# Kernel optimization log

Measured on AMD Instinct MI355X. Metric: run time of the kernel, lower is better.

## Reference

```python
import jax, jax.numpy as jnp
import numpy as np

D_MODEL = 1024
NUM_LAYERS = 4
D_STATE = 64
D_CONV = 4
EXPAND = 2
HEADDIM = 64  # headdim = d_state per the module
D_INNER = EXPAND * D_MODEL              # 2048
NHEADS = D_INNER // HEADDIM             # 32
CONV_DIM = D_INNER + 2 * D_STATE        # 2176 (x, B, C)
D_IN_PROJ = 2 * D_INNER + 2 * D_STATE + NHEADS  # 4384 (z, xBC, dt)
EPS = 1e-5


def setup_inputs() -> dict:
    key = jax.random.key(0)
    ks = jax.random.split(key, 8)
    B, L = 4, 2048
    x = jax.random.normal(ks[0], (B, L, D_MODEL), dtype=jnp.float32)
    # stacked per-layer parameters
    in_w = jax.random.normal(ks[1], (NUM_LAYERS, D_MODEL, D_IN_PROJ), dtype=jnp.float32) * 0.02
    conv_w = (jax.random.uniform(ks[2], (NUM_LAYERS, D_CONV, CONV_DIM), dtype=jnp.float32) - 0.5) * (2.0 / np.sqrt(D_CONV))
    conv_b = jnp.zeros((NUM_LAYERS, CONV_DIM), dtype=jnp.float32)
    # dt init as in mamba-ssm: dt ~ exp(U * (log(0.1)-log(0.001)) + log(0.001)), dt_bias = inv_softplus(dt)
    u = jax.random.uniform(ks[3], (NUM_LAYERS, NHEADS), dtype=jnp.float32)
    dt = jnp.exp(u * (np.log(0.1) - np.log(0.001)) + np.log(0.001))
    dt_bias = dt + jnp.log(-jnp.expm1(-dt))
    A_log = jnp.log(jax.random.uniform(ks[4], (NUM_LAYERS, NHEADS), dtype=jnp.float32, minval=1.0, maxval=16.0))
    Dp = jnp.ones((NUM_LAYERS, NHEADS), dtype=jnp.float32)
    norm_w = jnp.ones((NUM_LAYERS, D_INNER), dtype=jnp.float32)
    out_w = jax.random.normal(ks[5], (NUM_LAYERS, D_INNER, D_MODEL), dtype=jnp.float32) * 0.02
    ln_w = jnp.ones((NUM_LAYERS, D_MODEL), dtype=jnp.float32)
    ln_b = jnp.zeros((NUM_LAYERS, D_MODEL), dtype=jnp.float32)
    return {"x": x, "ln_w": ln_w, "ln_b": ln_b, "in_w": in_w, "conv_w": conv_w,
            "conv_b": conv_b, "dt_bias": dt_bias, "A_log": A_log, "Dp": Dp,
            "norm_w": norm_w, "out_w": out_w}


def _layernorm(x, w, b):
    mu = jnp.mean(x, axis=-1, keepdims=True)
    xc = x - mu
    var = jnp.mean(xc * xc, axis=-1, keepdims=True)
    return xc * jax.lax.rsqrt(var + EPS) * w + b


def _mamba2(x, in_w, conv_w, conv_b, dt_bias, A_log, Dp, norm_w, out_w):
    Bb, L, _ = x.shape
    zxbcdt = jnp.einsum('bld,de->ble', x, in_w)            # (B,L,D_IN_PROJ)
    z = zxbcdt[..., :D_INNER]                               # (B,L,D_INNER)
    xBC = zxbcdt[..., D_INNER:D_INNER + CONV_DIM]           # (B,L,CONV_DIM)
    dt = jax.nn.softplus(zxbcdt[..., -NHEADS:] + dt_bias)   # (B,L,H)
    # causal depthwise conv1d (kernel D_CONV) + SiLU
    xp = jnp.pad(xBC, ((0, 0), (D_CONV - 1, 0), (0, 0)))
    conv = conv_b + sum(xp[:, k:k + L, :] * conv_w[k] for k in range(D_CONV))
    xBC = jax.nn.silu(conv)
    xs = xBC[..., :D_INNER].reshape(Bb, L, NHEADS, HEADDIM)  # (B,L,H,P)
    Bm = xBC[..., D_INNER:D_INNER + D_STATE]                 # (B,L,N), ngroups=1
    Cm = xBC[..., D_INNER + D_STATE:]                        # (B,L,N)
    A = -jnp.exp(A_log)                                      # (H,)
    dA = jnp.exp(dt * A)                                     # (B,L,H) decay per step
    dBx = dt[..., None] * xs                                 # (B,L,H,P)
    # selective state-space scan: h_t = dA_t*h_{t-1} + dBx_t (x) B_t ; y_t = h_t . C_t
    def step(h, t_in):
        dA_t, dBx_t, B_t, C_t = t_in
        h = h * dA_t[:, :, None, None] + dBx_t[..., None] * B_t[:, None, None, :]
        y = jnp.einsum('bhpn,bn->bhp', h, C_t)
        return h, y
    h0 = jnp.zeros((Bb, NHEADS, HEADDIM, D_STATE), x.dtype)
    xsT = (jnp.moveaxis(dA, 1, 0), jnp.moveaxis(dBx, 1, 0),
           jnp.moveaxis(Bm, 1, 0), jnp.moveaxis(Cm, 1, 0))
    _, yT = jax.lax.scan(step, h0, xsT)
    y = jnp.moveaxis(yT, 0, 1)                               # (B,L,H,P)
    y = y + Dp[None, None, :, None] * xs                     # skip via per-head D
    y = y.reshape(Bb, L, D_INNER)
    # gated RMSNorm (norm_before_gate=False): rmsnorm(y * silu(z)) * w
    y = y * jax.nn.silu(z)
    y = y * jax.lax.rsqrt(jnp.mean(y * y, axis=-1, keepdims=True) + EPS) * norm_w
    return jnp.einsum('ble,ed->bld', y, out_w)


def reference(x, ln_w, ln_b, in_w, conv_w, conv_b, dt_bias, A_log, Dp, norm_w, out_w):
    for i in range(NUM_LAYERS):
        xn = _layernorm(x, ln_w[i], ln_b[i])
        x = x + _mamba2(xn, in_w[i], conv_w[i], conv_b[i], dt_bias[i],
                        A_log[i], Dp[i], norm_w[i], out_w[i])
    return x
```

## Files before the change

kernel.cpp:

```cpp
#include <hip/hip_runtime.h>
#include <math.h>

#define LSEQ   2048
#define NROWS  8192
#define DMODEL 1024
#define DINNER 2048
#define NH     32
#define CONVD  2176
#define NPROJ  4256
#define NPROJ_PAD 4352
#define EPSV   1e-5f
#define SEGS   16
#define TSEG   128

typedef __bf16 bf16x8_t __attribute__((ext_vector_type(8)));
typedef float f32x4_t __attribute__((ext_vector_type(4)));
typedef unsigned short u16x8_t __attribute__((ext_vector_type(8)));

__device__ __forceinline__ unsigned short f2bf(float f) {
  unsigned int u = __float_as_uint(f);
  u += 0x7fffu + ((u >> 16) & 1u);
  return (unsigned short)(u >> 16);
}
__device__ __forceinline__ float bf2f(unsigned short u) {
  return __uint_as_float((unsigned int)u << 16);
}
__device__ __forceinline__ float siluf(float x) { return x / (1.f + expf(-x)); }

__device__ __forceinline__ void gload16(const unsigned short* g, unsigned short* l) {
  __builtin_amdgcn_global_load_lds(
      (const __attribute__((address_space(1))) void*)g,
      (__attribute__((address_space(3))) void*)l, 16, 0, 0);
}

__global__ __launch_bounds__(256) void ln_kernel(const float* __restrict__ X,
    const float* __restrict__ w, const float* __restrict__ b,
    unsigned short* __restrict__ out)
{
  const int r = blockIdx.x, tid = threadIdx.x;
  __shared__ float red[4];
  const float4 v = ((const float4*)(X + (size_t)r * DMODEL))[tid];
  float s = v.x + v.y + v.z + v.w;
#pragma unroll
  for (int o = 32; o > 0; o >>= 1) s += __shfl_down(s, o);
  if ((tid & 63) == 0) red[tid >> 6] = s;
  __syncthreads();
  const float mu = (red[0] + red[1] + red[2] + red[3]) * (1.f / DMODEL);
  __syncthreads();
  const float dx = v.x - mu, dy = v.y - mu, dz = v.z - mu, dw = v.w - mu;
  float ss = dx * dx + dy * dy + dz * dz + dw * dw;
#pragma unroll
  for (int o = 32; o > 0; o >>= 1) ss += __shfl_down(ss, o);
  if ((tid & 63) == 0) red[tid >> 6] = ss;
  __syncthreads();
  const float var = (red[0] + red[1] + red[2] + red[3]) * (1.f / DMODEL);
  const float rs = rsqrtf(var + EPSV);
  const float4 wv = ((const float4*)w)[tid];
  const float4 bv = ((const float4*)b)[tid];
  const size_t d = (size_t)r * DMODEL + tid * 4;
  out[d + 0] = f2bf(dx * rs * wv.x + bv.x);
  out[d + 1] = f2bf(dy * rs * wv.y + bv.y);
  out[d + 2] = f2bf(dz * rs * wv.z + bv.z);
  out[d + 3] = f2bf(dw * rs * wv.w + bv.w);
}

__global__ void transpose_bf16(const float* __restrict__ W,
    unsigned short* __restrict__ WT, int K, int N)
{
  __shared__ float t[32][33];
  const int n0 = blockIdx.x * 32, k0 = blockIdx.y * 32;
  const int tx = threadIdx.x, ty = threadIdx.y;
  if (n0 + tx < N) t[ty][tx] = W[(size_t)(k0 + ty) * N + n0 + tx];
  __syncthreads();
  if (n0 + ty < N) WT[(size_t)(n0 + ty) * K + k0 + tx] = f2bf(t[tx][ty]);
}

__global__ __launch_bounds__(256) void gemm_bf16(
    const unsigned short* __restrict__ A,
    const unsigned short* __restrict__ BT,
    float* __restrict__ Cf,
    unsigned short* __restrict__ Cb,
    int N, int K, int ldc)
{
  __shared__ unsigned short sA[128 * 32];
  __shared__ unsigned short sB[128 * 32];
  const int tid = threadIdx.x;
  const int w = tid >> 6, l = tid & 63;
  const int wr = w >> 1, wc = w & 1;
  const int la = l & 15, lb = l >> 4;
  const int m0 = blockIdx.x * 128, n0 = blockIdx.y * 128;
  f32x4_t acc[4][4];
#pragma unroll
  for (int i = 0; i < 4; ++i)
#pragma unroll
    for (int j = 0; j < 4; ++j) acc[i][j] = (f32x4_t){0.f, 0.f, 0.f, 0.f};

  const int r0 = tid >> 2, q0 = tid & 3;
  const unsigned short* Ag = A + (size_t)(m0 + r0) * K + q0 * 8;
  const unsigned short* Bg = BT + (size_t)(n0 + r0) * K + q0 * 8;

  for (int kt = 0; kt < K; kt += 32) {
    __syncthreads();
    gload16(Ag + kt,                   sA + tid * 8);
    gload16(Ag + (size_t)64 * K + kt,  sA + 2048 + tid * 8);
    gload16(Bg + kt,                   sB + tid * 8);
    gload16(Bg + (size_t)64 * K + kt,  sB + 2048 + tid * 8);
    __syncthreads();
    bf16x8_t af[4], bfr[4];
#pragma unroll
    for (int mi = 0; mi < 4; ++mi)
      af[mi] = *(const bf16x8_t*)(sA + (wr * 64 + mi * 16 + la) * 32 + lb * 8);
#pragma unroll
    for (int ni = 0; ni < 4; ++ni)
      bfr[ni] = *(const bf16x8_t*)(sB + (wc * 64 + ni * 16 + la) * 32 + lb * 8);
#pragma unroll
    for (int mi = 0; mi < 4; ++mi)
#pragma unroll
      for (int ni = 0; ni < 4; ++ni)
        acc[mi][ni] = __builtin_amdgcn_mfma_f32_16x16x32_bf16(af[mi], bfr[ni], acc[mi][ni], 0, 0, 0);
  }
#pragma unroll
  for (int mi = 0; mi < 4; ++mi) {
#pragma unroll
    for (int ni = 0; ni < 4; ++ni) {
      const int col = n0 + wc * 64 + ni * 16 + la;
      if (col < N) {
#pragma unroll
        for (int r = 0; r < 4; ++r) {
          const int row = m0 + wr * 64 + mi * 16 + lb * 4 + r;
          const size_t idx = (size_t)row * ldc + col;
          const float v = acc[mi][ni][r];
          if (Cb) Cb[idx] = f2bf(v);
          else    Cf[idx] += v;
        }
      }
    }
  }
}

__global__ __launch_bounds__(256) void conv_kernel(const unsigned short* __restrict__ zx,
    const float* __restrict__ cw, const float* __restrict__ cb,
    unsigned short* __restrict__ out)
{
  const int c8 = (blockIdx.x * 256 + threadIdx.x) * 8;
  if (c8 >= CONVD) return;
  const int r = blockIdx.y;
  const int l = r & (LSEQ - 1);
  float acc[8];
  {
    const float4 b0 = *(const float4*)(cb + c8);
    const float4 b1 = *(const float4*)(cb + c8 + 4);
    acc[0] = b0.x; acc[1] = b0.y; acc[2] = b0.z; acc[3] = b0.w;
    acc[4] = b1.x; acc[5] = b1.y; acc[6] = b1.z; acc[7] = b1.w;
  }
#pragma unroll
  for (int k = 0; k < 4; ++k) {
    if (l + k - 3 >= 0) {
      const u16x8_t v = *(const u16x8_t*)(zx + (size_t)(r + k - 3) * NPROJ + DINNER + c8);
      const float4 w0 = *(const float4*)(cw + k * CONVD + c8);
      const float4 w1 = *(const float4*)(cw + k * CONVD + c8 + 4);
      acc[0] = fmaf(bf2f(v[0]), w0.x, acc[0]);
      acc[1] = fmaf(bf2f(v[1]), w0.y, acc[1]);
      acc[2] = fmaf(bf2f(v[2]), w0.z, acc[2]);
      acc[3] = fmaf(bf2f(v[3]), w0.w, acc[3]);
      acc[4] = fmaf(bf2f(v[4]), w1.x, acc[4]);
      acc[5] = fmaf(bf2f(v[5]), w1.y, acc[5]);
      acc[6] = fmaf(bf2f(v[6]), w1.z, acc[6]);
      acc[7] = fmaf(bf2f(v[7]), w1.w, acc[7]);
    }
  }
  u16x8_t o;
#pragma unroll
  for (int j = 0; j < 8; ++j) o[j] = f2bf(siluf(acc[j]));
  *(u16x8_t*)(out + (size_t)r * CONVD + c8) = o;
}

#define CBB(t, cbyte)  ((char*)CB  + (t) * 256 + ((cbyte) ^ (((t) & 7) << 4)))
#define XTB(p, cbyte)  ((char*)Xt  + (p) * 256 + ((cbyte) ^ (((p) & 7) << 4)))
#define BTWB(n, cbyte) ((char*)Btw + (n) * 256 + ((cbyte) ^ (((n) & 7) << 4)))
__global__ __launch_bounds__(256) void ssd_chunk_kernel(
    const unsigned short* __restrict__ xbc,
    const unsigned short* __restrict__ zraw,
    const float* __restrict__ dt_bias,
    const float* __restrict__ A_log,
    const float* __restrict__ Dp,
    unsigned short* __restrict__ y, int ldy,
    unsigned short* __restrict__ H,
    float* __restrict__ cumdec)
{
  __shared__ unsigned short CB[TSEG * 128];
  __shared__ unsigned short Xt[64 * TSEG];
  __shared__ unsigned short Btw[64 * TSEG];
  __shared__ float cumS[TSEG], dtS[TSEG], wS[TSEG];
  const int id = blockIdx.x;
  const int bh = id >> 4, ch = id & 15;
  const int b = bh >> 5, h = bh & 31;
  const int tid = threadIdx.x;
  const int w = tid >> 6, l = tid & 63;
  const int la = l & 15, lb = l >> 4;
  const size_t row0 = (size_t)b * LSEQ + (size_t)ch * TSEG;
  const unsigned short* xr = xbc + row0 * CONVD;
  const float dp = Dp[h];

  {
    const int t = tid >> 1, q = tid & 1;
    const unsigned short* src = xr + (size_t)t * CONVD;
#pragma unroll
    for (int j = 0; j < 4; ++j) {
      const int c0 = q * 32 + j * 8;
      *(u16x8_t*)CBB(t, c0 * 2)       = *(const u16x8_t*)(src + 2112 + c0);
      *(u16x8_t*)CBB(t, 128 + c0 * 2) = *(const u16x8_t*)(src + 2048 + c0);
      const u16x8_t xv = *(const u16x8_t*)(src + h * 64 + c0);
#pragma unroll
      for (int e = 0; e < 8; ++e)
        *(unsigned short*)XTB(c0 + e, t * 2) = xv[e];
    }
  }
  if (w == 0) {
    const float bias = dt_bias[h];
    const float aexp = __expf(A_log[h]);
    const float x0 = bf2f(zraw[(row0 + l) * NPROJ + (DINNER + CONVD) + h]) + bias;
    const float x1 = bf2f(zraw[(row0 + 64 + l) * NPROJ + (DINNER + CONVD) + h]) + bias;
    const float d0 = (x0 > 20.f) ? x0 : log1pf(__expf(x0));
    const float d1 = (x1 > 20.f) ? x1 : log1pf(__expf(x1));
    float a0 = -d0 * aexp;
    float a1 = -d1 * aexp;
#pragma unroll
    for (int o = 1; o < 64; o <<= 1) { const float u = __shfl_up(a0, o); if (l >= o) a0 += u; }
    const float tot0 = __shfl(a0, 63);
#pragma unroll
    for (int o = 1; o < 64; o <<= 1) { const float u = __shfl_up(a1, o); if (l >= o) a1 += u; }
    a1 += tot0;
    const float cT = __shfl(a1, 63);
    cumS[l] = a0;       cumS[64 + l] = a1;
    dtS[l] = d0;        dtS[64 + l] = d1;
    wS[l] = __expf(cT - a0) * d0;
    wS[64 + l] = __expf(cT - a1) * d1;
    float* cdg = cumdec + (size_t)bh * LSEQ + (size_t)ch * TSEG;
    cdg[l] = __expf(a0);
    cdg[64 + l] = __expf(a1);
  }
  __syncthreads();

  f32x4_t g[2][8];
#pragma unroll
  for (int mi = 0; mi < 2; ++mi)
#pragma unroll
    for (int ni = 0; ni < 8; ++ni) g[mi][ni] = (f32x4_t){0.f, 0.f, 0.f, 0.f};
#pragma unroll
  for (int ks = 0; ks < 2; ++ks) {
    bf16x8_t af[2], bfr[8];
#pragma unroll
    for (int mi = 0; mi < 2; ++mi)
      af[mi] = *(const bf16x8_t*)CBB(w * 32 + mi * 16 + la, ks * 64 + lb * 16);
#pragma unroll
    for (int ni = 0; ni < 8; ++ni)
      bfr[ni] = *(const bf16x8_t*)CBB(ni * 16 + la, 128 + ks * 64 + lb * 16);
#pragma unroll
    for (int mi = 0; mi < 2; ++mi)
#pragma unroll
      for (int ni = 0; ni < 8; ++ni)
        g[mi][ni] = __builtin_amdgcn_mfma_f32_16x16x32_bf16(af[mi], bfr[ni], g[mi][ni], 0, 0, 0);
  }
  __syncthreads();

#pragma unroll
  for (int mi = 0; mi < 2; ++mi) {
#pragma unroll
    for (int ni = 0; ni < 8; ++ni) {
      const int s = ni * 16 + la;
#pragma unroll
      for (int r = 0; r < 4; ++r) {
        const int t = w * 32 + mi * 16 + lb * 4 + r;
        float mv = 0.f;
        if (s <= t) mv = g[mi][ni][r] * __expf(cumS[t] - cumS[s]) * dtS[s];
        if (s == t) mv += dp;
        *(unsigned short*)CBB(t, s * 2) = f2bf(mv);
      }
    }
  }
  {
    const int s = tid >> 1, q = tid & 1;
    const unsigned short* src = xr + (size_t)s * CONVD + 2048;
    const float ww = wS[s];
#pragma unroll
    for (int j = 0; j < 4; ++j) {
      const int c0 = q * 32 + j * 8;
      const u16x8_t bv = *(const u16x8_t*)(src + c0);
#pragma unroll
      for (int e = 0; e < 8; ++e)
        *(unsigned short*)BTWB(c0 + e, s * 2) = f2bf(bf2f(bv[e]) * ww);
    }
  }
  __syncthreads();

  f32x4_t y1[2][4];
#pragma unroll
  for (int mi = 0; mi < 2; ++mi)
#pragma unroll
    for (int ni = 0; ni < 4; ++ni) y1[mi][ni] = (f32x4_t){0.f, 0.f, 0.f, 0.f};
#pragma unroll
  for (int ks = 0; ks < 4; ++ks) {
    bf16x8_t af[2], xf[4];
#pragma unroll
    for (int mi = 0; mi < 2; ++mi)
      af[mi] = *(const bf16x8_t*)CBB(w * 32 + mi * 16 + la, ks * 64 + lb * 16);
#pragma unroll
    for (int ni = 0; ni < 4; ++ni)
      xf[ni] = *(const bf16x8_t*)XTB(ni * 16 + la, ks * 64 + lb * 16);
#pragma unroll
    for (int mi = 0; mi < 2; ++mi)
#pragma unroll
      for (int ni = 0; ni < 4; ++ni)
        y1[mi][ni] = __builtin_amdgcn_mfma_f32_16x16x32_bf16(af[mi], xf[ni], y1[mi][ni], 0, 0, 0);
  }
  f32x4_t hacc[4];
#pragma unroll
  for (int ni = 0; ni < 4; ++ni) hacc[ni] = (f32x4_t){0.f, 0.f, 0.f, 0.f};
#pragma unroll
  for (int ks = 0; ks < 4; ++ks) {
    const bf16x8_t af = *(const bf16x8_t*)XTB(w * 16 + la, ks * 64 + lb * 16);
    bf16x8_t bw[4];
#pragma unroll
    for (int ni = 0; ni < 4; ++ni)
      bw[ni] = *(const bf16x8_t*)BTWB(ni * 16 + la, ks * 64 + lb * 16);
#pragma unroll
    for (int ni = 0; ni < 4; ++ni)
      hacc[ni] = __builtin_amdgcn_mfma_f32_16x16x32_bf16(af, bw[ni], hacc[ni], 0, 0, 0);
  }

  unsigned short* yg = y + row0 * ldy + h * 64;
#pragma unroll
  for (int mi = 0; mi < 2; ++mi)
#pragma unroll
    for (int ni = 0; ni < 4; ++ni)
#pragma unroll
      for (int r = 0; r < 4; ++r) {
        const int t = w * 32 + mi * 16 + lb * 4 + r;
        yg[(size_t)t * ldy + ni * 16 + la] = f2bf(y1[mi][ni][r]);
      }
  unsigned short* Hg = H + ((size_t)ch * 128 + bh) * 4096;
#pragma unroll
  for (int ni = 0; ni < 4; ++ni)
#pragma unroll
    for (int r = 0; r < 4; ++r) {
      const int p = w * 16 + lb * 4 + r;
      Hg[p * 64 + ni * 16 + la] = f2bf(hacc[ni][r]);
    }
}

__global__ __launch_bounds__(256) void scan2_kernel(
    unsigned short* __restrict__ H, const float* __restrict__ cumdec)
{
  const int bh = blockIdx.x;
  const int e = threadIdx.x * 16;
  float hs[16];
#pragma unroll
  for (int k = 0; k < 16; ++k) hs[k] = 0.f;
  unsigned short* Hb = H + (size_t)bh * 4096 + e;
  const float* cd = cumdec + (size_t)bh * LSEQ;
  for (int s = 0; s < SEGS; ++s) {
    unsigned short* p = Hb + (size_t)s * 128 * 4096;
    const float rseg = cd[s * TSEG + TSEG - 1];
    u16x8_t v0 = *(u16x8_t*)p, v1 = *(u16x8_t*)(p + 8);
    u16x8_t w0, w1;
#pragma unroll
    for (int k = 0; k < 8; ++k) {
      const float tmp = bf2f(v0[k]);
      w0[k] = f2bf(hs[k]);
      hs[k] = fmaf(rseg, hs[k], tmp);
    }
#pragma unroll
    for (int k = 0; k < 8; ++k) {
      const float tmp = bf2f(v1[k]);
      w1[k] = f2bf(hs[k + 8]);
      hs[k + 8] = fmaf(rseg, hs[k + 8], tmp);
    }
    *(u16x8_t*)p = w0;
    *(u16x8_t*)(p + 8) = w1;
  }
}

#define CSB(t, cbyte) ((char*)Cs + (t) * 128 + ((cbyte) ^ (((t) & 7) << 4)))
#define HSB(p, cbyte) ((char*)Hs + (p) * 128 + ((cbyte) ^ (((p) & 7) << 4)))
__global__ __launch_bounds__(256) void scan3_mfma(
    const unsigned short* __restrict__ xbc,
    const float* __restrict__ cumdec,
    const unsigned short* __restrict__ H,
    unsigned short* __restrict__ y, int ldy)
{
  __shared__ unsigned short Cs[TSEG * 64];
  __shared__ unsigned short Hs[64 * 64];
  __shared__ float cdS[TSEG];
  const int id = blockIdx.x;
  const int bh = id / 15, ch = id % 15 + 1;
  const int b = bh >> 5, h = bh & 31;
  const int tid = threadIdx.x, w = tid >> 6, l = tid & 63;
  const int la = l & 15, lb = l >> 4;
  const size_t row0 = (size_t)b * LSEQ + (size_t)ch * TSEG;
  const unsigned short* xr = xbc + row0 * CONVD;
  {
    const int t = tid >> 1, q = tid & 1;
#pragma unroll
    for (int j = 0; j < 4; ++j) {
      const int c0 = q * 32 + j * 8;
      *(u16x8_t*)CSB(t, c0 * 2) = *(const u16x8_t*)(xr + (size_t)t * CONVD + 2112 + c0);
    }
  }
  {
    const int p = tid >> 2, q = tid & 3;
    const unsigned short* hsrc = H + ((size_t)ch * 128 + bh) * 4096 + p * 64;
#pragma unroll
    for (int j = 0; j < 2; ++j) {
      const int c0 = q * 16 + j * 8;
      *(u16x8_t*)HSB(p, c0 * 2) = *(const u16x8_t*)(hsrc + c0);
    }
  }
  if (tid < TSEG) cdS[tid] = cumdec[(size_t)bh * LSEQ + (size_t)ch * TSEG + tid];
  __syncthreads();
  f32x4_t acc[2][4];
#pragma unroll
  for (int mi = 0; mi < 2; ++mi)
#pragma unroll
    for (int ni = 0; ni < 4; ++ni) acc[mi][ni] = (f32x4_t){0.f, 0.f, 0.f, 0.f};
#pragma unroll
  for (int ks = 0; ks < 2; ++ks) {
    bf16x8_t af[2], bfr[4];
#pragma unroll
    for (int mi = 0; mi < 2; ++mi)
      af[mi] = *(const bf16x8_t*)CSB(w * 32 + mi * 16 + la, ks * 64 + lb * 16);
#pragma unroll
    for (int ni = 0; ni < 4; ++ni)
      bfr[ni] = *(const bf16x8_t*)HSB(ni * 16 + la, ks * 64 + lb * 16);
#pragma unroll
    for (int mi = 0; mi < 2; ++mi)
#pragma unroll
      for (int ni = 0; ni < 4; ++ni)
        acc[mi][ni] = __builtin_amdgcn_mfma_f32_16x16x32_bf16(af[mi], bfr[ni], acc[mi][ni], 0, 0, 0);
  }
  unsigned short* yg = y + row0 * ldy + h * 64;
#pragma unroll
  for (int mi = 0; mi < 2; ++mi)
#pragma unroll
    for (int ni = 0; ni < 4; ++ni)
#pragma unroll
      for (int r = 0; r < 4; ++r) {
        const int t = w * 32 + mi * 16 + lb * 4 + r;
        unsigned short* yp = yg + (size_t)t * ldy + ni * 16 + la;
        *yp = f2bf(bf2f(*yp) + acc[mi][ni][r] * cdS[t]);
      }
}

__global__ __launch_bounds__(256) void gate_kernel(const unsigned short* __restrict__ zx,
    const float* __restrict__ nw, unsigned short* __restrict__ out)
{
  const int r = blockIdx.x, tid = threadIdx.x;
  __shared__ float red[4];
  const size_t rb = (size_t)r * NPROJ;
  const u16x8_t zv = *(const u16x8_t*)(zx + rb + tid * 8);
  const u16x8_t yv = *(const u16x8_t*)(zx + rb + 2048 + tid * 8);
  float v[8];
#pragma unroll
  for (int i = 0; i < 8; ++i) v[i] = bf2f(yv[i]) * siluf(bf2f(zv[i]));
  float ss = 0.f;
#pragma unroll
  for (int i = 0; i < 8; ++i) ss += v[i] * v[i];
#pragma unroll
  for (int o = 32; o > 0; o >>= 1) ss += __shfl_down(ss, o);
  if ((tid & 63) == 0) red[tid >> 6] = ss;
  __syncthreads();
  const float var = (red[0] + red[1] + red[2] + red[3]) * (1.f / DINNER);
  const float rs = rsqrtf(var + EPSV);
  const float4 w0 = ((const float4*)nw)[tid * 2];
  const float4 w1 = ((const float4*)nw)[tid * 2 + 1];
  u16x8_t o;
  o[0] = f2bf(v[0] * rs * w0.x); o[1] = f2bf(v[1] * rs * w0.y);
  o[2] = f2bf(v[2] * rs * w0.z); o[3] = f2bf(v[3] * rs * w0.w);
  o[4] = f2bf(v[4] * rs * w1.x); o[5] = f2bf(v[5] * rs * w1.y);
  o[6] = f2bf(v[6] * rs * w1.z); o[7] = f2bf(v[7] * rs * w1.w);
  *(u16x8_t*)(out + (size_t)r * DINNER + tid * 8) = o;
}

extern "C" void kernel_launch(void* const* d_in, const int* in_sizes, int n_in,
                              void* d_out, int out_size, void* d_ws, size_t ws_size,
                              hipStream_t stream) {
  (void)in_sizes; (void)n_in; (void)out_size; (void)ws_size;
  const float* x_in    = (const float*)d_in[0];
  const float* ln_w    = (const float*)d_in[1];
  const float* ln_b    = (const float*)d_in[2];
  const float* in_w    = (const float*)d_in[3];
  const float* conv_w  = (const float*)d_in[4];
  const float* conv_b  = (const float*)d_in[5];
  const float* dt_bias = (const float*)d_in[6];
  const float* A_log   = (const float*)d_in[7];
  const float* Dp      = (const float*)d_in[8];
  const float* norm_w  = (const float*)d_in[9];
  const float* out_w   = (const float*)d_in[10];
  float* xout = (float*)d_out;

  char* ws = (char*)d_ws;
  unsigned short* zxb  = (unsigned short*)ws;
  char* r1 = ws + (size_t)NROWS * NPROJ * 2;
  unsigned short* xn   = (unsigned short*)r1;
  unsigned short* xbcb = (unsigned short*)r1;
  unsigned short* ybf  = (unsigned short*)r1;
  char* wth = r1 + (size_t)NROWS * CONVD * 2;
  unsigned short* inwT = (unsigned short*)wth;
  unsigned short* owT  = (unsigned short*)wth;
  unsigned short* Hbuf = (unsigned short*)wth;
  float* cumdec = (float*)(wth + (size_t)SEGS * 128 * 4096 * 2);

  hipMemcpyAsync(xout, x_in, (size_t)NROWS * DMODEL * 4, hipMemcpyDeviceToDevice, stream);

  for (int i = 0; i < 4; ++i) {
    ln_kernel<<<NROWS, 256, 0, stream>>>(xout, ln_w + i * DMODEL, ln_b + i * DMODEL, xn);
    transpose_bf16<<<dim3(133, 32), dim3(32, 32), 0, stream>>>(
        in_w + (size_t)i * DMODEL * NPROJ, inwT, DMODEL, NPROJ);
    gemm_bf16<<<dim3(64, 34), 256, 0, stream>>>(xn, inwT, nullptr, zxb, NPROJ, DMODEL, NPROJ);
    conv_kernel<<<dim3(2, NROWS), 256, 0, stream>>>(
        zxb, conv_w + (size_t)i * 4 * CONVD, conv_b + i * CONVD, xbcb);
    ssd_chunk_kernel<<<128 * SEGS, 256, 0, stream>>>(xbcb, zxb,
        dt_bias + i * NH, A_log + i * NH, Dp + i * NH,
        zxb + 2048, NPROJ, Hbuf, cumdec);
    scan2_kernel<<<128, 256, 0, stream>>>(Hbuf, cumdec);
    scan3_mfma<<<128 * 15, 256, 0, stream>>>(xbcb, cumdec, Hbuf, zxb + 2048, NPROJ);
    gate_kernel<<<NROWS, 256, 0, stream>>>(zxb, norm_w + i * DINNER, ybf);
    transpose_bf16<<<dim3(32, 64), dim3(32, 32), 0, stream>>>(
        out_w + (size_t)i * DINNER * DMODEL, owT, DINNER, DMODEL);
    gemm_bf16<<<dim3(64, 8), 256, 0, stream>>>(ybf, owT, xout, nullptr, DMODEL, DINNER, DMODEL);
  }
}
```

Measured before the change: 1.414 ms.

## Double-buffer LDS tiles in bf16 GEMM to overlap loads with MFMA

Splits the GEMM's shared-memory A/B tiles into two buffers and software-pipelines the K loop, so the global-to-LDS load for the next K step is issued before the MFMAs on the current step. This removes one of the two barriers per iteration and hides load latency behind compute. It doubles LDS use per block, which may lower occupancy, and it assumes K/32 is even (the loop processes two tiles per iteration and always stages t+1).

```diff
diff --git a/kernel.cpp b/kernel.cpp
--- a/kernel.cpp
+++ b/kernel.cpp
@@ -75,6 +75,36 @@
   if (n0 + ty < N) WT[(size_t)(n0 + ty) * K + k0 + tx] = f2bf(t[tx][ty]);
 }
 
+#define STAGE(BUF, KT) do {                                        \
+    const int kt_ = (KT) * 32;                                     \
+    gload16(Ag + kt_,                  sA##BUF + tid * 8);         \
+    gload16(Ag + (size_t)64 * K + kt_, sA##BUF + 2048 + tid * 8);  \
+    gload16(Bg + kt_,                  sB##BUF + tid * 8);         \
+    gload16(Bg + (size_t)64 * K + kt_, sB##BUF + 2048 + tid * 8);  \
+  } while (0)
+
+#define COMPUTE(BUF) do {                                                           \
+    bf16x8_t af[4], bfr[4];                                                         \
+    _Pragma("unroll")                                                               \
+    for (int mi = 0; mi < 4; ++mi)                                                  \
+      af[mi] = *(const bf16x8_t*)(sA##BUF + (wr * 64 + mi * 16 + la) * 32 + lb * 8);\
+    _Pragma("unroll")                                                               \
+    for (int ni = 0; ni < 4; ++ni)                                                  \
+      bfr[ni] = *(const bf16x8_t*)(sB##BUF + (wc * 64 + ni * 16 + la) * 32 + lb * 8);\
+    _Pragma("unroll")                                                               \
+    for (int mi = 0; mi < 4; ++mi)                                                  \
+      _Pragma("unroll")                                                             \
+      for (int ni = 0; ni < 4; ++ni)                                                \
+        acc[mi][ni] = __builtin_amdgcn_mfma_f32_16x16x32_bf16(af[mi], bfr[ni],      \
+                                                              acc[mi][ni], 0, 0, 0);\
+  } while (0)
+
+#define SYNC_PIPE do {                                   \
+    __builtin_amdgcn_sched_barrier(0);                   \
+    asm volatile("s_waitcnt vmcnt(0)" ::: "memory");     \
+    __builtin_amdgcn_s_barrier();                        \
+  } while (0)
+
 __global__ __launch_bounds__(256) void gemm_bf16(
     const unsigned short* __restrict__ A,
     const unsigned short* __restrict__ BT,
@@ -82,8 +112,10 @@
     unsigned short* __restrict__ Cb,
     int N, int K, int ldc)
 {
-  __shared__ unsigned short sA[128 * 32];
-  __shared__ unsigned short sB[128 * 32];
+  __shared__ __attribute__((aligned(16))) unsigned short sA0[128 * 32];
+  __shared__ __attribute__((aligned(16))) unsigned short sA1[128 * 32];
+  __shared__ __attribute__((aligned(16))) unsigned short sB0[128 * 32];
+  __shared__ __attribute__((aligned(16))) unsigned short sB1[128 * 32];
   const int tid = threadIdx.x;
   const int w = tid >> 6, l = tid & 63;
   const int wr = w >> 1, wc = w & 1;
@@ -98,27 +130,20 @@
   const int r0 = tid >> 2, q0 = tid & 3;
   const unsigned short* Ag = A + (size_t)(m0 + r0) * K + q0 * 8;
   const unsigned short* Bg = BT + (size_t)(n0 + r0) * K + q0 * 8;
-
-  for (int kt = 0; kt < K; kt += 32) {
-    __syncthreads();
-    gload16(Ag + kt,                   sA + tid * 8);
-    gload16(Ag + (size_t)64 * K + kt,  sA + 2048 + tid * 8);
-    gload16(Bg + kt,                   sB + tid * 8);
-    gload16(Bg + (size_t)64 * K + kt,  sB + 2048 + tid * 8);
-    __syncthreads();
-    bf16x8_t af[4], bfr[4];
-#pragma unroll
-    for (int mi = 0; mi < 4; ++mi)
-      af[mi] = *(const bf16x8_t*)(sA + (wr * 64 + mi * 16 + la) * 32 + lb * 8);
-#pragma unroll
-    for (int ni = 0; ni < 4; ++ni)
-      bfr[ni] = *(const bf16x8_t*)(sB + (wc * 64 + ni * 16 + la) * 32 + lb * 8);
-#pragma unroll
-    for (int mi = 0; mi < 4; ++mi)
-#pragma unroll
-      for (int ni = 0; ni < 4; ++ni)
-        acc[mi][ni] = __builtin_amdgcn_mfma_f32_16x16x32_bf16(af[mi], bfr[ni], acc[mi][ni], 0, 0, 0);
-  }
+  const int nkt = K / 32;
+
+  STAGE(0, 0);
+  SYNC_PIPE;
+
+  for (int t = 0; t < nkt; t += 2) {
+    STAGE(1, t + 1);
+    COMPUTE(0);
+    SYNC_PIPE;
+    if (t + 2 < nkt) STAGE(0, t + 2);
+    COMPUTE(1);
+    SYNC_PIPE;
+  }
+
 #pragma unroll
   for (int mi = 0; mi < 4; ++mi) {
 #pragma unroll
```

Result: slower. 1.481 ms (+4.7%).
